# Performance work log

Measured on AMD Instinct MI355X. Metric: run time of the kernel, lower is better.

## Reference

```python
import jax, jax.numpy as jnp
import numpy as np

COMMITMENT_COST = 0.25


def setup_inputs() -> dict:
    key = jax.random.key(0)
    k1, k2 = jax.random.split(key)
    inputs = jax.random.normal(k1, (16, 256, 64, 64), dtype=jnp.float32)
    embed = jax.random.normal(k2, (1024, 256), dtype=jnp.float32)
    return {"inputs": inputs, "embed": embed}


def _l4_dist_pow(flat, embed):
    # torch.cdist(flat, embed, p=ndim) with ndim=4 -> argmin of sum_d (x-e)^4.
    # cross terms are plain [N,D]@[D,K] GEMMs (no [N,K,D] intermediate).
    x2 = flat * flat
    x3 = x2 * flat
    x4 = x3 * flat
    e = embed
    e2 = e * e
    e3 = e2 * e
    e4 = e3 * e
    d = (x4.sum(-1, keepdims=True)
         + e4.sum(-1)[None, :]
         + 6.0 * (x2 @ e2.T)
         - 4.0 * (x3 @ e.T)
         - 4.0 * (flat @ e3.T))
    return d  # [N, K], equals cdist(...)**4; argmin is unchanged by the 4th root


def reference(inputs, embed):
    # inputs: [B, C, H, W] with C == embedding_dim; eval-mode forward (no EMA update)
    C = embed.shape[1]
    x = jnp.moveaxis(inputs, 1, -1)            # [B, H, W, C] (channel_last)
    input_shape = x.shape
    flat = x.reshape(-1, C)                    # [N, C]

    dist = _l4_dist_pow(flat, embed)           # [N, K]
    encoding_indices = jnp.argmin(dist, axis=1)  # [N]

    quantized = embed[encoding_indices].reshape(input_shape)  # gather
    quantized = jnp.moveaxis(quantized, -1, 1)                # back to [B, C, H, W]
    quantized = jax.lax.stop_gradient(quantized)

    e_latent_loss = jnp.mean((quantized - inputs) ** 2)
    loss = COMMITMENT_COST * e_latent_loss

    # straight-through estimator
    quantized_st = inputs + jax.lax.stop_gradient(quantized - inputs)
    encoding_indices = encoding_indices.reshape(input_shape[:-1])  # [B, H, W]
    return quantized_st, encoding_indices, loss
```

## Files before the change

### kernel.cpp

```cpp
#include <hip/hip_runtime.h>
#include <stdint.h>

#define DIM 256
#define HWSZ 4096
#define N_ROWS 65536
#define KCB 1024
#define Q_ELEMS 16777216
#define COMMIT 0.25f

typedef __attribute__((ext_vector_type(8))) _Float16 f16x8;
typedef __attribute__((ext_vector_type(4))) float f32x4;

#define OFF_BH   0u
#define OFF_BL   1572864u
#define OFF_BIAS 3145728u
#define OFF_CVAL 3149824u
#define OFF_CIDX 7344128u
#define OFF_IDX  11538432u
#define OFF_LOSS 11800576u

#define MFMA(a, b, c) __builtin_amdgcn_mfma_f32_16x16x32_f16(a, b, c, 0, 0, 0)

__device__ __forceinline__ void splitf16(float p, unsigned& hbits, unsigned& lbits) {
    const _Float16 h = (_Float16)p;
    const float hf = (float)h;
    const _Float16 l = (_Float16)(p - hf);
    hbits = (unsigned)__builtin_bit_cast(unsigned short, h);
    lbits = (unsigned)__builtin_bit_cast(unsigned short, l);
}

__device__ __forceinline__ void glds16(const unsigned short* src, unsigned short* dst) {
    __builtin_amdgcn_global_load_lds((const __attribute__((address_space(1))) void*)src,
                                     (__attribute__((address_space(3))) void*)dst, 16, 0, 0);
}

__global__ void prep_embed(const float* __restrict__ embed,
                           unsigned short* __restrict__ Bh, unsigned short* __restrict__ Bl,
                           float* __restrict__ bias, float* __restrict__ loss) {
    const int col = blockIdx.x, c = threadIdx.x;
    const float e = embed[col * DIM + c];
    const float e2 = e * e, e3 = e2 * e, e4 = e2 * e2;
    const float wv[3] = {-4.f * e3, 6.f * e2, -4.f * e};
    const int g = (c >> 3) & 3, j = c & 7, kb = c & 0xE0;
    const int swz = (col >> 1) & 3;
    #pragma unroll
    for (int s = 0; s < 3; ++s) {
        unsigned hb, lb;
        splitf16(wv[s], hb, lb);
        const int pos = col * 768 + s * 256 + kb + ((g ^ swz) << 3) + j;
        Bh[pos] = (unsigned short)hb;
        Bl[pos] = (unsigned short)lb;
    }
    __shared__ float red[256];
    red[c] = e4;
    __syncthreads();
    for (int o = 128; o > 0; o >>= 1) { if (c < o) red[c] += red[c + o]; __syncthreads(); }
    if (c == 0) { bias[col] = red[0]; if (col == 0) *loss = 0.f; }
}

__launch_bounds__(256, 2)
__global__ void dist_mfma(const float* __restrict__ x,
                          const unsigned short* __restrict__ Bh,
                          const unsigned short* __restrict__ Bl,
                          const float* __restrict__ bias,
                          float* __restrict__ cval, int* __restrict__ cidx) {
    __shared__ __align__(16) unsigned char smem[32768];
    char* As_h = (char*)smem;
    char* As_l = (char*)smem + 8192;
    char* Bs_h = (char*)smem + 16384;
    char* Bs_l = (char*)smem + 24576;

    const int t = threadIdx.x;
    const int rowblk = blockIdx.x >> 3, colblk = blockIdx.x & 7;
    const int n0 = rowblk << 7;
    const float* xb = x + (((size_t)(n0 >> 12)) << 20) + (n0 & 4095);

    const int w = t >> 6, l = t & 63;
    const int lr = l & 15, lg = l >> 4;
    const int wrow = (w >> 1) << 6, wcol = (w & 1) << 6;

    int aoff[4], boff[4];
    #pragma unroll
    for (int mi = 0; mi < 4; ++mi) {
        const int row = wrow + mi * 16 + lr;
        aoff[mi] = row * 64 + ((lg ^ ((row >> 1) & 3)) << 4);
    }
    #pragma unroll
    for (int ni = 0; ni < 4; ++ni) {
        const int cl = wcol + ni * 16 + lr;
        boff[ni] = cl * 64 + ((lg ^ ((cl >> 1) & 3)) << 4);
    }

    const int sm = t & 127, cg = t >> 7;
    const int aswz = (sm >> 1) & 3;
    const int wo0 = (sm << 6) + (((cg * 2 + 0) ^ aswz) << 4);
    const int wo1 = (sm << 6) + (((cg * 2 + 1) ^ aswz) << 4);

    const int bcol = t >> 2, bk16 = t & 3;
    const size_t bgbase = (size_t)(colblk * 128 + bcol) * 768 + bk16 * 8;
    unsigned short* ldsBh0 = (unsigned short*)Bs_h + t * 8;
    unsigned short* ldsBh1 = (unsigned short*)Bs_h + 2048 + t * 8;
    unsigned short* ldsBl0 = (unsigned short*)Bs_l + t * 8;
    unsigned short* ldsBl1 = (unsigned short*)Bs_l + 2048 + t * 8;

    f32x4 acc[4][4];
    #pragma unroll
    for (int mi = 0; mi < 4; ++mi)
        #pragma unroll
        for (int ni = 0; ni < 4; ++ni) acc[mi][ni] = (f32x4){0.f, 0.f, 0.f, 0.f};

    #pragma unroll 1
    for (int kk = 0; kk < 24; ++kk) {
        const int cc = kk / 3;
        const int s  = kk - cc * 3;
        const int kgl = s * 256 + cc * 32;

        glds16(Bh + bgbase + kgl, ldsBh0);
        glds16(Bh + bgbase + (size_t)64 * 768 + kgl, ldsBh1);
        glds16(Bl + bgbase + kgl, ldsBl0);
        glds16(Bl + bgbase + (size_t)64 * 768 + kgl, ldsBl1);

        const float* xc = xb + (((size_t)(cc * 32 + cg * 16)) << 12) + sm;
        #pragma unroll
        for (int half = 0; half < 2; ++half) {
            unsigned hw_[4], lw_[4];
            #pragma unroll
            for (int jp = 0; jp < 4; ++jp) {
                const float v0 = xc[(size_t)(half * 8 + jp * 2) << 12];
                const float v1 = xc[(size_t)(half * 8 + jp * 2 + 1) << 12];
                float p0 = v0, p1 = v1;
                if (s >= 1) { p0 *= v0; p1 *= v1; }
                if (s == 2) { p0 *= v0; p1 *= v1; }
                unsigned h0, l0, h1, l1;
                splitf16(p0, h0, l0);
                splitf16(p1, h1, l1);
                hw_[jp] = h0 | (h1 << 16);
                lw_[jp] = l0 | (l1 << 16);
            }
            const int wo = half ? wo1 : wo0;
            *(uint4*)(As_h + wo) = make_uint4(hw_[0], hw_[1], hw_[2], hw_[3]);
            *(uint4*)(As_l + wo) = make_uint4(lw_[0], lw_[1], lw_[2], lw_[3]);
        }
        __syncthreads();

        f16x8 vbh[4], vbl[4];
        #pragma unroll
        for (int ni = 0; ni < 4; ++ni) {
            vbh[ni] = *(const f16x8*)(Bs_h + boff[ni]);
            vbl[ni] = *(const f16x8*)(Bs_l + boff[ni]);
        }
        #pragma unroll
        for (int mi = 0; mi < 4; ++mi) {
            const f16x8 ah = *(const f16x8*)(As_h + aoff[mi]);
            const f16x8 al = *(const f16x8*)(As_l + aoff[mi]);
            #pragma unroll
            for (int ni = 0; ni < 4; ++ni) {
                acc[mi][ni] = MFMA(ah, vbh[ni], acc[mi][ni]);
                acc[mi][ni] = MFMA(al, vbh[ni], acc[mi][ni]);
                acc[mi][ni] = MFMA(ah, vbl[ni], acc[mi][ni]);
            }
        }
        __syncthreads();
    }

    const int colbase = colblk * 128 + wcol;
    float bs[4];
    #pragma unroll
    for (int ni = 0; ni < 4; ++ni) bs[ni] = bias[colbase + ni * 16 + lr];
    const int slot = colblk * 2 + (w & 1);
    #pragma unroll
    for (int mi = 0; mi < 4; ++mi) {
        #pragma unroll
        for (int r = 0; r < 4; ++r) {
            float bv = acc[mi][0][r] + bs[0];
            int bi = colbase + lr;
            #pragma unroll
            for (int ni = 1; ni < 4; ++ni) {
                const float v2 = acc[mi][ni][r] + bs[ni];
                if (v2 < bv) { bv = v2; bi = colbase + ni * 16 + lr; }
            }
            #pragma unroll
            for (int o = 1; o < 16; o <<= 1) {
                const float ov = __shfl_xor(bv, o, 64);
                const int oi = __shfl_xor(bi, o, 64);
                if (ov < bv || (ov == bv && oi < bi)) { bv = ov; bi = oi; }
            }
            if (lr == 0) {
                const int n = n0 + wrow + mi * 16 + lg * 4 + r;
                cval[slot * N_ROWS + n] = bv;
                cidx[slot * N_ROWS + n] = bi;
            }
        }
    }
}

__global__ void reduce_argmin(const float* __restrict__ cval, const int* __restrict__ cidx,
                              int* __restrict__ idx) {
    const int n = blockIdx.x * 256 + threadIdx.x;
    float bv = cval[n];
    int bi = cidx[n];
    #pragma unroll
    for (int s = 1; s < 16; ++s) {
        const float v = cval[s * N_ROWS + n];
        const int i = cidx[s * N_ROWS + n];
        if (v < bv || (v == bv && i < bi)) { bv = v; bi = i; }
    }
    idx[n] = bi;
}

__global__ void gather_out(const float* __restrict__ x, const float* __restrict__ embed,
                           const int* __restrict__ idx, float* __restrict__ out,
                           float* __restrict__ loss_accum) {
    const int tid = blockIdx.x * blockDim.x + threadIdx.x;
    const int g = tid << 2;
    const int bq = g >> 20;
    const int c = (g >> 12) & 255;
    const int hw = g & 4095;
    const int n = (bq << 12) | hw;

    const int4 id4 = *(const int4*)(idx + n);
    const float4 xv = *(const float4*)(x + g);
    float4 q;
    q.x = embed[id4.x * DIM + c];
    q.y = embed[id4.y * DIM + c];
    q.z = embed[id4.z * DIM + c];
    q.w = embed[id4.w * DIM + c];
    float4 d;
    d.x = q.x - xv.x; d.y = q.y - xv.y; d.z = q.z - xv.z; d.w = q.w - xv.w;
    float4 st;
    st.x = xv.x + d.x; st.y = xv.y + d.y; st.z = xv.z + d.z; st.w = xv.w + d.w;
    *(float4*)(out + g) = st;

    float ls = d.x * d.x + d.y * d.y + d.z * d.z + d.w * d.w;
    #pragma unroll
    for (int o = 32; o > 0; o >>= 1) ls += __shfl_down(ls, o, 64);
    __shared__ float ps[4];
    if ((threadIdx.x & 63) == 0) ps[threadIdx.x >> 6] = ls;
    __syncthreads();
    if (threadIdx.x == 0) atomicAdd(loss_accum, ps[0] + ps[1] + ps[2] + ps[3]);

    if (tid < N_ROWS / 4) {
        const int4 iv = *(const int4*)(idx + (tid << 2));
        float4 f;
        f.x = (float)iv.x; f.y = (float)iv.y; f.z = (float)iv.z; f.w = (float)iv.w;
        *(float4*)(out + Q_ELEMS + (tid << 2)) = f;
    }
}

__global__ void finalize_loss(const float* __restrict__ loss_accum, float* __restrict__ out) {
    out[Q_ELEMS + N_ROWS] = COMMIT * (*loss_accum) / (float)Q_ELEMS;
}

extern "C" void kernel_launch(void* const* d_in, const int* in_sizes, int n_in,
                              void* d_out, int out_size, void* d_ws, size_t ws_size,
                              hipStream_t stream) {
    const float* x = (const float*)d_in[0];
    const float* embed = (const float*)d_in[1];
    char* ws = (char*)d_ws;
    unsigned short* Bh = (unsigned short*)(ws + OFF_BH);
    unsigned short* Bl = (unsigned short*)(ws + OFF_BL);
    float* bias = (float*)(ws + OFF_BIAS);
    float* cval = (float*)(ws + OFF_CVAL);
    int* cidx = (int*)(ws + OFF_CIDX);
    int* idx = (int*)(ws + OFF_IDX);
    float* lacc = (float*)(ws + OFF_LOSS);
    float* out = (float*)d_out;

    hipLaunchKernelGGL(prep_embed, dim3(KCB), dim3(DIM), 0, stream, embed, Bh, Bl, bias, lacc);
    hipLaunchKernelGGL(dist_mfma, dim3(4096), dim3(256), 0, stream, x, Bh, Bl, bias, cval, cidx);
    hipLaunchKernelGGL(reduce_argmin, dim3(N_ROWS / 256), dim3(256), 0, stream, cval, cidx, idx);
    hipLaunchKernelGGL(gather_out, dim3(Q_ELEMS / 4 / 256), dim3(256), 0, stream, x, embed, idx, out, lacc);
    hipLaunchKernelGGL(finalize_loss, dim3(1), dim3(1), 0, stream, lacc, out);
}
```

Measured before the change: 659.2 us.

## Precompute fp16 split powers of x into workspace tiles; double-buffer GEMM loads

Adds a convert_x kernel that computes x, x^2 and x^3, splits each into fp16 hi/lo parts and stores them in a pre-swizzled tile layout. This runs in four passes of 16384 rows so the workspace footprint stays bounded. The distance kernel then loads both A and B tiles with direct global-to-LDS loads into a double-buffered 64KB shared buffer, replacing per-iteration register conversion of strided fp32 x. This trades extra workspace traffic and launches for a cheaper, overlapped GEMM inner loop. gather_out also now handles four float4 chunks per thread, which cuts block count and atomics.

```diff
diff --git a/kernel.cpp b/kernel.cpp
--- a/kernel.cpp
+++ b/kernel.cpp
@@ -7,6 +7,7 @@
 #define KCB 1024
 #define Q_ELEMS 16777216
 #define COMMIT 0.25f
+#define PASS_ROWS 16384
 
 typedef __attribute__((ext_vector_type(8))) _Float16 f16x8;
 typedef __attribute__((ext_vector_type(4))) float f32x4;
@@ -18,6 +19,9 @@
 #define OFF_CIDX 7344128u
 #define OFF_IDX  11538432u
 #define OFF_LOSS 11800576u
+#define OFF_AH   11800832u
+#define OFF_AL   36966656u
+#define WS_NEED  62132480ull
 
 #define MFMA(a, b, c) __builtin_amdgcn_mfma_f32_16x16x32_f16(a, b, c, 0, 0, 0)
 
@@ -58,12 +62,172 @@
     if (c == 0) { bias[col] = red[0]; if (col == 0) *loss = 0.f; }
 }
 
+__global__ void convert_x(const float* __restrict__ x, int passBase,
+                          unsigned short* __restrict__ Ah, unsigned short* __restrict__ Al) {
+    const int t = threadIdx.x;
+    const int sm = t & 63, q = t >> 6;
+    const int b = blockIdx.x;
+    const int n = passBase + b * 64 + sm;
+    const int rit = ((b & 1) << 6) + sm;
+    const int rbl = b >> 1;
+    const float* xp = x + (((size_t)(n >> 12)) << 20) + (n & 4095);
+    const int swz = (rit >> 1) & 3;
+
+    #pragma unroll
+    for (int h2 = 0; h2 < 2; ++h2) {
+        const int cc = q * 2 + h2;
+        float xv[32], pw[32];
+        #pragma unroll
+        for (int j = 0; j < 32; ++j) {
+            xv[j] = xp[(size_t)(cc * 32 + j) << 12];
+            pw[j] = xv[j];
+        }
+        #pragma unroll
+        for (int s = 0; s < 3; ++s) {
+            if (s) {
+                #pragma unroll
+                for (int j = 0; j < 32; ++j) pw[j] *= xv[j];
+            }
+            const int kk = cc * 3 + s;
+            const size_t base = (((size_t)(rbl * 24 + kk)) * 128 + rit) * 32;
+            #pragma unroll
+            for (int g = 0; g < 4; ++g) {
+                unsigned hw_[4], lw_[4];
+                #pragma unroll
+                for (int e = 0; e < 4; ++e) {
+                    unsigned h0, l0, h1, l1;
+                    splitf16(pw[g * 8 + 2 * e], h0, l0);
+                    splitf16(pw[g * 8 + 2 * e + 1], h1, l1);
+                    hw_[e] = h0 | (h1 << 16);
+                    lw_[e] = l0 | (l1 << 16);
+                }
+                const int go = (g ^ swz) << 3;
+                *(uint4*)(Ah + base + go) = make_uint4(hw_[0], hw_[1], hw_[2], hw_[3]);
+                *(uint4*)(Al + base + go) = make_uint4(lw_[0], lw_[1], lw_[2], lw_[3]);
+            }
+        }
+    }
+}
+
 __launch_bounds__(256, 2)
-__global__ void dist_mfma(const float* __restrict__ x,
+__global__ void dist_mfma(const unsigned short* __restrict__ Ah,
+                          const unsigned short* __restrict__ Al,
                           const unsigned short* __restrict__ Bh,
                           const unsigned short* __restrict__ Bl,
-                          const float* __restrict__ bias,
+                          const float* __restrict__ bias, int passBase,
                           float* __restrict__ cval, int* __restrict__ cidx) {
+    __shared__ __align__(16) unsigned char smem[65536];
+
+    const int t = threadIdx.x;
+    const int rbl = blockIdx.x >> 3, colblk = blockIdx.x & 7;
+    const int n0 = passBase + (rbl << 7);
+
+    const int w = t >> 6, l = t & 63;
+    const int lr = l & 15, lg = l >> 4;
+    const int wrow = (w >> 1) << 6, wcol = (w & 1) << 6;
+
+    int aoff[4], boff[4];
+    #pragma unroll
+    for (int mi = 0; mi < 4; ++mi) {
+        const int row = wrow + mi * 16 + lr;
+        aoff[mi] = row * 64 + ((lg ^ ((row >> 1) & 3)) << 4);
+    }
+    #pragma unroll
+    for (int ni = 0; ni < 4; ++ni) {
+        const int cl = wcol + ni * 16 + lr;
+        boff[ni] = 16384 + cl * 64 + ((lg ^ ((cl >> 1) & 3)) << 4);
+    }
+
+    const int bcol = t >> 2;
+    const size_t bsrc0 = (size_t)(colblk * 128 + bcol) * 768 + (t & 3) * 8;
+    const size_t bsrc1 = bsrc0 + (size_t)64 * 768;
+    const size_t atileBase = (size_t)rbl * 24 * 4096;
+
+    auto stage = [&](int kk, int buf) {
+        const int cc = kk / 3, s = kk - cc * 3;
+        const int kgl = s * 256 + cc * 32;
+        unsigned short* base = (unsigned short*)(smem + (buf << 15));
+        const unsigned short* ah = Ah + atileBase + (size_t)kk * 4096;
+        const unsigned short* al = Al + atileBase + (size_t)kk * 4096;
+        glds16(ah + t * 8, base + t * 8);
+        glds16(ah + 2048 + t * 8, base + 2048 + t * 8);
+        glds16(al + t * 8, base + 4096 + t * 8);
+        glds16(al + 2048 + t * 8, base + 4096 + 2048 + t * 8);
+        glds16(Bh + bsrc0 + kgl, base + 8192 + t * 8);
+        glds16(Bh + bsrc1 + kgl, base + 8192 + 2048 + t * 8);
+        glds16(Bl + bsrc0 + kgl, base + 12288 + t * 8);
+        glds16(Bl + bsrc1 + kgl, base + 12288 + 2048 + t * 8);
+    };
+
+    f32x4 acc[4][4];
+    #pragma unroll
+    for (int mi = 0; mi < 4; ++mi)
+        #pragma unroll
+        for (int ni = 0; ni < 4; ++ni) acc[mi][ni] = (f32x4){0.f, 0.f, 0.f, 0.f};
+
+    stage(0, 0);
+    #pragma unroll 1
+    for (int kk = 0; kk < 24; ++kk) {
+        __syncthreads();
+        if (kk < 23) stage(kk + 1, (kk + 1) & 1);
+        const int bofs = (kk & 1) << 15;
+
+        f16x8 vbh[4], vbl[4];
+        #pragma unroll
+        for (int ni = 0; ni < 4; ++ni) {
+            vbh[ni] = *(const f16x8*)(smem + bofs + boff[ni]);
+            vbl[ni] = *(const f16x8*)(smem + bofs + boff[ni] + 8192);
+        }
+        #pragma unroll
+        for (int mi = 0; mi < 4; ++mi) {
+            const f16x8 ah = *(const f16x8*)(smem + bofs + aoff[mi]);
+            const f16x8 al = *(const f16x8*)(smem + bofs + aoff[mi] + 8192);
+            #pragma unroll
+            for (int ni = 0; ni < 4; ++ni) {
+                acc[mi][ni] = MFMA(ah, vbh[ni], acc[mi][ni]);
+                acc[mi][ni] = MFMA(al, vbh[ni], acc[mi][ni]);
+                acc[mi][ni] = MFMA(ah, vbl[ni], acc[mi][ni]);
+            }
+        }
+    }
+
+    const int colbase = colblk * 128 + wcol;
+    float bs[4];
+    #pragma unroll
+    for (int ni = 0; ni < 4; ++ni) bs[ni] = bias[colbase + ni * 16 + lr];
+    const int slot = colblk * 2 + (w & 1);
+    #pragma unroll
+    for (int mi = 0; mi < 4; ++mi) {
+        #pragma unroll
+        for (int r = 0; r < 4; ++r) {
+            float bv = acc[mi][0][r] + bs[0];
+            int bi = colbase + lr;
+            #pragma unroll
+            for (int ni = 1; ni < 4; ++ni) {
+                const float v2 = acc[mi][ni][r] + bs[ni];
+                if (v2 < bv) { bv = v2; bi = colbase + ni * 16 + lr; }
+            }
+            #pragma unroll
+            for (int o = 1; o < 16; o <<= 1) {
+                const float ov = __shfl_xor(bv, o, 64);
+                const int oi = __shfl_xor(bi, o, 64);
+                if (ov < bv || (ov == bv && oi < bi)) { bv = ov; bi = oi; }
+            }
+            if (lr == 0) {
+                const int n = n0 + wrow + mi * 16 + lg * 4 + r;
+                cval[slot * N_ROWS + n] = bv;
+                cidx[slot * N_ROWS + n] = bi;
+            }
+        }
+    }
+}
+
+__launch_bounds__(256, 2)
+__global__ void dist_mfma_fb(const float* __restrict__ x,
+                             const unsigned short* __restrict__ Bh,
+                             const unsigned short* __restrict__ Bl,
+                             const float* __restrict__ bias,
+                             float* __restrict__ cval, int* __restrict__ cidx) {
     __shared__ __align__(16) unsigned char smem[32768];
     char* As_h = (char*)smem;
     char* As_l = (char*)smem + 8192;
@@ -96,8 +260,8 @@
     const int wo0 = (sm << 6) + (((cg * 2 + 0) ^ aswz) << 4);
     const int wo1 = (sm << 6) + (((cg * 2 + 1) ^ aswz) << 4);
 
-    const int bcol = t >> 2, bk16 = t & 3;
-    const size_t bgbase = (size_t)(colblk * 128 + bcol) * 768 + bk16 * 8;
+    const int bcol = t >> 2;
+    const size_t bgbase = (size_t)(colblk * 128 + bcol) * 768 + (t & 3) * 8;
     unsigned short* ldsBh0 = (unsigned short*)Bs_h + t * 8;
     unsigned short* ldsBh1 = (unsigned short*)Bs_h + 2048 + t * 8;
     unsigned short* ldsBl0 = (unsigned short*)Bs_l + t * 8;
@@ -112,7 +276,7 @@
     #pragma unroll 1
     for (int kk = 0; kk < 24; ++kk) {
         const int cc = kk / 3;
-        const int s  = kk - cc * 3;
+        const int s = kk - cc * 3;
         const int kgl = s * 256 + cc * 32;
 
         glds16(Bh + bgbase + kgl, ldsBh0);
@@ -211,27 +375,31 @@
 __global__ void gather_out(const float* __restrict__ x, const float* __restrict__ embed,
                            const int* __restrict__ idx, float* __restrict__ out,
                            float* __restrict__ loss_accum) {
-    const int tid = blockIdx.x * blockDim.x + threadIdx.x;
-    const int g = tid << 2;
-    const int bq = g >> 20;
-    const int c = (g >> 12) & 255;
-    const int hw = g & 4095;
-    const int n = (bq << 12) | hw;
-
-    const int4 id4 = *(const int4*)(idx + n);
-    const float4 xv = *(const float4*)(x + g);
-    float4 q;
-    q.x = embed[id4.x * DIM + c];
-    q.y = embed[id4.y * DIM + c];
-    q.z = embed[id4.z * DIM + c];
-    q.w = embed[id4.w * DIM + c];
-    float4 d;
-    d.x = q.x - xv.x; d.y = q.y - xv.y; d.z = q.z - xv.z; d.w = q.w - xv.w;
-    float4 st;
-    st.x = xv.x + d.x; st.y = xv.y + d.y; st.z = xv.z + d.z; st.w = xv.w + d.w;
-    *(float4*)(out + g) = st;
-
-    float ls = d.x * d.x + d.y * d.y + d.z * d.z + d.w * d.w;
+    const int gtid = blockIdx.x * 256 + threadIdx.x;
+    float ls = 0.f;
+    #pragma unroll
+    for (int it = 0; it < 4; ++it) {
+        const int tid = gtid + it * 1048576;
+        const int g = tid << 2;
+        const int bq = g >> 20;
+        const int c = (g >> 12) & 255;
+        const int hw = g & 4095;
+        const int n = (bq << 12) | hw;
+
+        const int4 id4 = *(const int4*)(idx + n);
+        const float4 xv = *(const float4*)(x + g);
+        float4 q;
+        q.x = embed[id4.x * DIM + c];
+        q.y = embed[id4.y * DIM + c];
+        q.z = embed[id4.z * DIM + c];
+        q.w = embed[id4.w * DIM + c];
+        float4 d;
+        d.x = q.x - xv.x; d.y = q.y - xv.y; d.z = q.z - xv.z; d.w = q.w - xv.w;
+        float4 st;
+        st.x = xv.x + d.x; st.y = xv.y + d.y; st.z = xv.z + d.z; st.w = xv.w + d.w;
+        *(float4*)(out + g) = st;
+        ls += d.x * d.x + d.y * d.y + d.z * d.z + d.w * d.w;
+    }
     #pragma unroll
     for (int o = 32; o > 0; o >>= 1) ls += __shfl_down(ls, o, 64);
     __shared__ float ps[4];
@@ -239,11 +407,11 @@
     __syncthreads();
     if (threadIdx.x == 0) atomicAdd(loss_accum, ps[0] + ps[1] + ps[2] + ps[3]);
 
-    if (tid < N_ROWS / 4) {
-        const int4 iv = *(const int4*)(idx + (tid << 2));
+    if (gtid < N_ROWS / 4) {
+        const int4 iv = *(const int4*)(idx + (gtid << 2));
         float4 f;
         f.x = (float)iv.x; f.y = (float)iv.y; f.z = (float)iv.z; f.w = (float)iv.w;
-        *(float4*)(out + Q_ELEMS + (tid << 2)) = f;
+        *(float4*)(out + Q_ELEMS + (gtid << 2)) = f;
     }
 }
 
@@ -264,11 +432,23 @@
     int* cidx = (int*)(ws + OFF_CIDX);
     int* idx = (int*)(ws + OFF_IDX);
     float* lacc = (float*)(ws + OFF_LOSS);
+    unsigned short* Ah = (unsigned short*)(ws + OFF_AH);
+    unsigned short* Al = (unsigned short*)(ws + OFF_AL);
     float* out = (float*)d_out;
 
     hipLaunchKernelGGL(prep_embed, dim3(KCB), dim3(DIM), 0, stream, embed, Bh, Bl, bias, lacc);
-    hipLaunchKernelGGL(dist_mfma, dim3(4096), dim3(256), 0, stream, x, Bh, Bl, bias, cval, cidx);
+    if (ws_size >= WS_NEED) {
+        for (int p = 0; p < 4; ++p) {
+            hipLaunchKernelGGL(convert_x, dim3(PASS_ROWS / 64), dim3(256), 0, stream,
+                               x, p * PASS_ROWS, Ah, Al);
+            hipLaunchKernelGGL(dist_mfma, dim3((PASS_ROWS / 128) * 8), dim3(256), 0, stream,
+                               Ah, Al, Bh, Bl, bias, p * PASS_ROWS, cval, cidx);
+        }
+    } else {
+        hipLaunchKernelGGL(dist_mfma_fb, dim3(4096), dim3(256), 0, stream,
+                           x, Bh, Bl, bias, cval, cidx);
+    }
     hipLaunchKernelGGL(reduce_argmin, dim3(N_ROWS / 256), dim3(256), 0, stream, cval, cidx, idx);
-    hipLaunchKernelGGL(gather_out, dim3(Q_ELEMS / 4 / 256), dim3(256), 0, stream, x, embed, idx, out, lacc);
+    hipLaunchKernelGGL(gather_out, dim3(4096), dim3(256), 0, stream, x, embed, idx, out, lacc);
     hipLaunchKernelGGL(finalize_loss, dim3(1), dim3(1), 0, stream, lacc, out);
 }
```

Result: faster. 572.2 us (-13.2%).
